# Optimization experiments

Measured on AMD Instinct MI355X. Metric: run time of the kernel, lower is better.

The kernel has to match this reference:

```python
import jax, jax.numpy as jnp
import numpy as np

N_HEADS = 8
EMBED_DIM = 512
HEAD_DIM = EMBED_DIM // N_HEADS
INPUT_DIM = 512


def setup_inputs() -> dict:
    key = jax.random.key(0)
    ks = jax.random.split(key, 9)
    B, N = 4, 2048
    s_in = 1.0 / np.sqrt(INPUT_DIM)
    s_e = 1.0 / np.sqrt(EMBED_DIM)
    return {
        "q": jax.random.normal(ks[0], (B, N, INPUT_DIM), dtype=jnp.float32),
        "wq": jax.random.uniform(ks[1], (EMBED_DIM, INPUT_DIM), jnp.float32, -s_in, s_in),
        "bq": jax.random.uniform(ks[2], (EMBED_DIM,), jnp.float32, -s_in, s_in),
        "wk": jax.random.uniform(ks[3], (EMBED_DIM, INPUT_DIM), jnp.float32, -s_in, s_in),
        "bk": jax.random.uniform(ks[4], (EMBED_DIM,), jnp.float32, -s_in, s_in),
        "wv": jax.random.uniform(ks[5], (EMBED_DIM, INPUT_DIM), jnp.float32, -s_in, s_in),
        "bv": jax.random.uniform(ks[6], (EMBED_DIM,), jnp.float32, -s_in, s_in),
        "wo": jax.random.uniform(ks[7], (EMBED_DIM, EMBED_DIM), jnp.float32, -s_e, s_e),
        "bo": jax.random.uniform(ks[8], (EMBED_DIM,), jnp.float32, -s_e, s_e),
    }


def reference(q, wq, bq, wk, bk, wv, bv, wo, bo):
    B, N, _ = q.shape
    # linear projections (torch Linear: x @ W.T + b)
    Q = (q @ wq.T + bq).reshape(B, N, N_HEADS, HEAD_DIM).transpose(0, 2, 1, 3)
    K = (q @ wk.T + bk).reshape(B, N, N_HEADS, HEAD_DIM).transpose(0, 2, 1, 3)
    V = (q @ wv.T + bv).reshape(B, N, N_HEADS, HEAD_DIM).transpose(0, 2, 1, 3)
    scores = jnp.einsum("bhqd,bhkd->bhqk", Q, K) / jnp.sqrt(
        jnp.asarray(HEAD_DIM, dtype=q.dtype)
    )
    weights = jax.nn.softmax(scores, axis=-1)
    out = jnp.einsum("bhqk,bhkd->bhqd", weights, V)  # [B,H,N,Dh]
    out = out.transpose(0, 2, 1, 3).reshape(B, N, EMBED_DIM)
    return out @ wo.T + bo
```

## Files before the change

### kernel.cpp

```cpp
#include <hip/hip_runtime.h>
#include <hip/hip_bf16.h>
#include <math.h>

#define SEQ    2048
#define DH     64
#define EMB    512
#define INDIM  512
#define NHEADS 8
#define BATCH  4
#define MTOT   (BATCH * SEQ)

typedef __attribute__((ext_vector_type(8))) short bf16x8;
typedef __attribute__((ext_vector_type(4))) float f32x4;

__device__ __forceinline__ ushort f2bf(float x) {
  union { float f; unsigned u; } v; v.f = x;
  unsigned r = v.u + 0x7FFFu + ((v.u >> 16) & 1u);
  return (ushort)(r >> 16);
}

__device__ __forceinline__ unsigned cvt_pk_bf16(float lo, float hi) {
  unsigned r;
  asm("v_cvt_pk_bf16_f32 %0, %1, %2" : "=v"(r) : "v"(lo), "v"(hi));
  return r;
}

__device__ __forceinline__ float fast_exp2(float x) {
  float r;
  asm("v_exp_f32 %0, %1" : "=v"(r) : "v"(x));
  return r;
}

__device__ __forceinline__ void permswap32(unsigned &x, unsigned &y) {
  asm("v_permlane32_swap_b32 %0, %1" : "+v"(x), "+v"(y));
}

__global__ __launch_bounds__(256) void conv_bf16(const float* __restrict__ src,
                                                 ushort* __restrict__ dst, int n8) {
  const int i = blockIdx.x * 256 + threadIdx.x;
  if (i >= n8) return;
  const float4 a = ((const float4*)src)[i * 2];
  const float4 b = ((const float4*)src)[i * 2 + 1];
  uint4 o;
  o.x = cvt_pk_bf16(a.x, a.y);
  o.y = cvt_pk_bf16(a.z, a.w);
  o.z = cvt_pk_bf16(b.x, b.y);
  o.w = cvt_pk_bf16(b.z, b.w);
  ((uint4*)dst)[i] = o;
}

__global__ __launch_bounds__(256) void conv_bf16_w4(
    const float* __restrict__ w0, const float* __restrict__ w1,
    const float* __restrict__ w2, const float* __restrict__ w3,
    ushort* __restrict__ dst, int n8per) {
  const int i = blockIdx.x * 256 + threadIdx.x;
  if (i >= n8per) return;
  const float* src = (blockIdx.y == 0) ? w0 : (blockIdx.y == 1) ? w1
                   : (blockIdx.y == 2) ? w2 : w3;
  ushort* d = dst + (size_t)blockIdx.y * n8per * 8;
  const float4 a = ((const float4*)src)[i * 2];
  const float4 b = ((const float4*)src)[i * 2 + 1];
  uint4 o;
  o.x = cvt_pk_bf16(a.x, a.y);
  o.y = cvt_pk_bf16(a.z, a.w);
  o.z = cvt_pk_bf16(b.x, b.y);
  o.w = cvt_pk_bf16(b.z, b.w);
  ((uint4*)d)[i] = o;
}

template <int MODE>
__global__ __launch_bounds__(256) void mfma_gemm(
    const ushort* __restrict__ A, const ushort* __restrict__ W,
    const float* __restrict__ b0, const float* __restrict__ b1,
    const float* __restrict__ b2,
    ushort* __restrict__ outQ, ushort* __restrict__ outK,
    ushort* __restrict__ outVT, float* __restrict__ outF) {
  __shared__ __align__(16) char smem[MODE == 0 ? 35840 : 16384];
  ushort* As = (ushort*)smem;
  ushort* Bs = (ushort*)(smem + 8192);
  ushort* Tl = (ushort*)smem;

  const int bm = blockIdx.x * 128;
  const int bn = blockIdx.y * 128;
  const int tid = threadIdx.x;
  const int wave = tid >> 6, lane = tid & 63;
  const int g = lane >> 4, ln = lane & 15;
  const int wr = wave >> 1, wc = wave & 1;

  f32x4 acc[4][4];
#pragma unroll
  for (int m = 0; m < 4; ++m)
#pragma unroll
    for (int n = 0; n < 4; ++n) acc[m][n] = (f32x4){0.f, 0.f, 0.f, 0.f};

  const size_t a_base = (size_t)(bm + wave * 16 + (lane >> 2)) * INDIM + (lane & 3) * 8;
  const size_t b_base = (size_t)(bn + wave * 16 + (lane >> 2)) * INDIM + (lane & 3) * 8;
  ushort* ldsA0 = As + wave * 512;
  ushort* ldsA1 = As + 2048 + wave * 512;
  ushort* ldsB0 = Bs + wave * 512;
  ushort* ldsB1 = Bs + 2048 + wave * 512;

  for (int k0 = 0; k0 < INDIM; k0 += 32) {
    __syncthreads();
    __builtin_amdgcn_global_load_lds(
        (const __attribute__((address_space(1))) void*)(A + a_base + k0),
        (__attribute__((address_space(3))) void*)ldsA0, 16, 0, 0);
    __builtin_amdgcn_global_load_lds(
        (const __attribute__((address_space(1))) void*)(A + a_base + 64 * INDIM + k0),
        (__attribute__((address_space(3))) void*)ldsA1, 16, 0, 0);
    __builtin_amdgcn_global_load_lds(
        (const __attribute__((address_space(1))) void*)(W + b_base + k0),
        (__attribute__((address_space(3))) void*)ldsB0, 16, 0, 0);
    __builtin_amdgcn_global_load_lds(
        (const __attribute__((address_space(1))) void*)(W + b_base + 64 * INDIM + k0),
        (__attribute__((address_space(3))) void*)ldsB1, 16, 0, 0);
    __syncthreads();

    bf16x8 af[4], bfv[4];
#pragma unroll
    for (int m = 0; m < 4; ++m)
      af[m] = *(const bf16x8*)&As[(64 * wr + 16 * m + ln) * 32 + 8 * g];
#pragma unroll
    for (int n = 0; n < 4; ++n)
      bfv[n] = *(const bf16x8*)&Bs[(64 * wc + 16 * n + ln) * 32 + 8 * g];
#pragma unroll
    for (int m = 0; m < 4; ++m)
#pragma unroll
      for (int n = 0; n < 4; ++n)
        acc[m][n] = __builtin_amdgcn_mfma_f32_16x16x32_bf16(af[m], bfv[n], acc[m][n], 0, 0, 0);
  }

  if (MODE == 1) {
#pragma unroll
    for (int n = 0; n < 4; ++n) {
      const int e = bn + 64 * wc + 16 * n + ln;
      const float bv = b0[e];
#pragma unroll
      for (int m = 0; m < 4; ++m)
#pragma unroll
        for (int r = 0; r < 4; ++r) {
          const int row = bm + 64 * wr + 16 * m + 4 * g + r;
          outF[(size_t)row * EMB + e] = acc[m][n][r] + bv;
        }
    }
    return;
  }

  const int which = bn >> 9;
  const float* bias = (which == 0) ? b0 : (which == 1) ? b1 : b2;

  if (which < 2) {
    const float scl = (which == 0) ? 0.18033688f : 1.0f;
    ushort* dst = (which == 0) ? outQ : outK;
#pragma unroll
    for (int n = 0; n < 4; ++n) {
      const int e = (bn & 511) + 64 * wc + 16 * n + ln;
      const float bv = bias[e];
      const int h = e >> 6, d = e & 63;
#pragma unroll
      for (int m = 0; m < 4; ++m)
#pragma unroll
        for (int r = 0; r < 4; ++r) {
          const int row = bm + 64 * wr + 16 * m + 4 * g + r;
          const int b = row >> 11, nn = row & (SEQ - 1);
          dst[(((size_t)(b * NHEADS + h) * SEQ) + nn) * DH + d] =
              f2bf((acc[m][n][r] + bv) * scl);
        }
    }
  } else {
    __syncthreads();
#pragma unroll
    for (int n = 0; n < 4; ++n) {
      const int cl = 64 * wc + 16 * n + ln;
      const float bv = bias[(bn & 511) + cl];
#pragma unroll
      for (int m = 0; m < 4; ++m)
#pragma unroll
        for (int r = 0; r < 4; ++r) {
          const int rl = 64 * wr + 16 * m + 4 * g + r;
          Tl[cl * 140 + rl] = f2bf(acc[m][n][r] + bv);
        }
    }
    __syncthreads();
    const int c = tid >> 1;
    const int rh = (tid & 1) * 64;
    const int e = (bn & 511) + c;
    const int h = e >> 6, d = e & 63;
    const int b = bm >> 11;
    const int nn0 = (bm & (SEQ - 1)) + rh;
    ushort* drow = outVT + (((size_t)(b * NHEADS + h) * DH) + d) * SEQ + nn0;
#pragma unroll
    for (int j = 0; j < 8; ++j)
      *(bf16x8*)&drow[j * 8] = *(const bf16x8*)&Tl[c * 140 + rh + j * 8];
  }
}

__global__ __launch_bounds__(256) void attn_mfma(const ushort* __restrict__ Q,
                                                 const ushort* __restrict__ K,
                                                 const ushort* __restrict__ VT,
                                                 ushort* __restrict__ O) {
  __shared__ __align__(16) ushort Kl[64 * 72];
  __shared__ __align__(16) ushort Vl[64 * 72];

  const int tid = threadIdx.x;
  const int wave = tid >> 6, lane = tid & 63;
  const int g = lane >> 4, ln = lane & 15;

  const int orig = blockIdx.x;
  const int swz = (orig & 7) * 64 + (orig >> 3);
  const int bh = swz >> 4;
  const int qx = swz & 15;
  const int qbase = qx * 128 + wave * 32;

  const ushort* Qb = Q + ((size_t)bh * SEQ + qbase) * DH;
  const ushort* Kb = K + (size_t)bh * SEQ * DH;
  const ushort* Vb = VT + (size_t)bh * DH * SEQ;

  const bf16x8 qfA0 = *(const bf16x8*)&Qb[ln * DH + 8 * g];
  const bf16x8 qfA1 = *(const bf16x8*)&Qb[ln * DH + 32 + 8 * g];
  const bf16x8 qfB0 = *(const bf16x8*)&Qb[(16 + ln) * DH + 8 * g];
  const bf16x8 qfB1 = *(const bf16x8*)&Qb[(16 + ln) * DH + 32 + 8 * g];

  f32x4 oaccA[4], oaccB[4];
#pragma unroll
  for (int t = 0; t < 4; ++t) {
    oaccA[t] = (f32x4){0.f, 0.f, 0.f, 0.f};
    oaccB[t] = (f32x4){0.f, 0.f, 0.f, 0.f};
  }
  float denomA = 0.f, denomB = 0.f;

  const int skv = tid >> 3, sd = (tid & 7) * 8;
  const int dt = tid >> 2, kc = (tid & 3) * 8;
  const int pr0 = skv ^ (((((skv >> 2) ^ (skv >> 3)) & 1)) * 12);
  const int s32 = skv + 32;
  const int pr1 = s32 ^ (((((s32 >> 2) ^ (s32 >> 3)) & 1)) * 12);

  bf16x8 k0v = *(const bf16x8*)&Kb[(size_t)skv * DH + sd];
  bf16x8 k1v = *(const bf16x8*)&Kb[(size_t)(32 + skv) * DH + sd];
  bf16x8 v0v = *(const bf16x8*)&Vb[(size_t)dt * SEQ + kc];
  bf16x8 v1v = *(const bf16x8*)&Vb[(size_t)dt * SEQ + 32 + kc];

  for (int kv0 = 0; kv0 < SEQ; kv0 += 64) {
    __syncthreads();
    *(bf16x8*)&Kl[pr0 * 72 + sd] = k0v;
    *(bf16x8*)&Kl[pr1 * 72 + sd] = k1v;
    *(bf16x8*)&Vl[dt * 72 + kc] = v0v;
    *(bf16x8*)&Vl[dt * 72 + 32 + kc] = v1v;

    const int nxt = (kv0 + 64 < SEQ) ? kv0 + 64 : kv0;
    k0v = *(const bf16x8*)&Kb[(size_t)(nxt + skv) * DH + sd];
    k1v = *(const bf16x8*)&Kb[(size_t)(nxt + 32 + skv) * DH + sd];
    v0v = *(const bf16x8*)&Vb[(size_t)dt * SEQ + nxt + kc];
    v1v = *(const bf16x8*)&Vb[(size_t)dt * SEQ + nxt + 32 + kc];

    asm volatile("s_waitcnt lgkmcnt(0)" ::: "memory");
    __builtin_amdgcn_s_barrier();

    bf16x8 ka[4][2], vb[2][4];
#pragma unroll
    for (int t = 0; t < 4; ++t) {
      ka[t][0] = *(const bf16x8*)&Kl[(16 * t + ln) * 72 + 8 * g];
      ka[t][1] = *(const bf16x8*)&Kl[(16 * t + ln) * 72 + 32 + 8 * g];
    }
#pragma unroll
    for (int c = 0; c < 2; ++c)
#pragma unroll
      for (int t = 0; t < 4; ++t)
        vb[c][t] = *(const bf16x8*)&Vl[(16 * t + ln) * 72 + 32 * c + 8 * g];

    {
      f32x4 s0 = (f32x4){0.f, 0.f, 0.f, 0.f};
      f32x4 s1 = s0, s2 = s0, s3 = s0;
      __builtin_amdgcn_s_setprio(1);
      s0 = __builtin_amdgcn_mfma_f32_16x16x32_bf16(ka[0][0], qfA0, s0, 0, 0, 0);
      s1 = __builtin_amdgcn_mfma_f32_16x16x32_bf16(ka[1][0], qfA0, s1, 0, 0, 0);
      s2 = __builtin_amdgcn_mfma_f32_16x16x32_bf16(ka[2][0], qfA0, s2, 0, 0, 0);
      s3 = __builtin_amdgcn_mfma_f32_16x16x32_bf16(ka[3][0], qfA0, s3, 0, 0, 0);
      s0 = __builtin_amdgcn_mfma_f32_16x16x32_bf16(ka[0][1], qfA1, s0, 0, 0, 0);
      s1 = __builtin_amdgcn_mfma_f32_16x16x32_bf16(ka[1][1], qfA1, s1, 0, 0, 0);
      s2 = __builtin_amdgcn_mfma_f32_16x16x32_bf16(ka[2][1], qfA1, s2, 0, 0, 0);
      s3 = __builtin_amdgcn_mfma_f32_16x16x32_bf16(ka[3][1], qfA1, s3, 0, 0, 0);
      __builtin_amdgcn_s_setprio(0);

      float p0[4], p1[4], p2[4], p3[4];
#pragma unroll
      for (int r = 0; r < 4; ++r) {
        p0[r] = fast_exp2(s0[r]);
        p1[r] = fast_exp2(s1[r]);
        p2[r] = fast_exp2(s2[r]);
        p3[r] = fast_exp2(s3[r]);
      }
      float ds = ((p0[0] + p0[1]) + (p0[2] + p0[3]))
               + ((p1[0] + p1[1]) + (p1[2] + p1[3]))
               + ((p2[0] + p2[1]) + (p2[2] + p2[3]))
               + ((p3[0] + p3[1]) + (p3[2] + p3[3]));
      ds += __shfl_xor(ds, 16);
      ds += __shfl_xor(ds, 32);
      denomA += ds;

      unsigned a0 = cvt_pk_bf16(p0[0], p0[1]);
      unsigned a2 = cvt_pk_bf16(p1[0], p1[1]);
      unsigned a1 = cvt_pk_bf16(p0[2], p0[3]);
      unsigned a3 = cvt_pk_bf16(p1[2], p1[3]);
      permswap32(a0, a2);
      permswap32(a1, a3);
      unsigned b0 = cvt_pk_bf16(p2[0], p2[1]);
      unsigned b2 = cvt_pk_bf16(p3[0], p3[1]);
      unsigned b1 = cvt_pk_bf16(p2[2], p2[3]);
      unsigned b3 = cvt_pk_bf16(p3[2], p3[3]);
      permswap32(b0, b2);
      permswap32(b1, b3);
      union { unsigned u[4]; bf16x8 v; } pa0, pa1;
      pa0.u[0] = a0; pa0.u[1] = a1; pa0.u[2] = a2; pa0.u[3] = a3;
      pa1.u[0] = b0; pa1.u[1] = b1; pa1.u[2] = b2; pa1.u[3] = b3;

      __builtin_amdgcn_s_setprio(1);
#pragma unroll
      for (int t = 0; t < 4; ++t) {
        oaccA[t] = __builtin_amdgcn_mfma_f32_16x16x32_bf16(pa0.v, vb[0][t], oaccA[t], 0, 0, 0);
        oaccA[t] = __builtin_amdgcn_mfma_f32_16x16x32_bf16(pa1.v, vb[1][t], oaccA[t], 0, 0, 0);
      }
      __builtin_amdgcn_s_setprio(0);
    }

    {
      f32x4 s0 = (f32x4){0.f, 0.f, 0.f, 0.f};
      f32x4 s1 = s0, s2 = s0, s3 = s0;
      __builtin_amdgcn_s_setprio(1);
      s0 = __builtin_amdgcn_mfma_f32_16x16x32_bf16(ka[0][0], qfB0, s0, 0, 0, 0);
      s1 = __builtin_amdgcn_mfma_f32_16x16x32_bf16(ka[1][0], qfB0, s1, 0, 0, 0);
      s2 = __builtin_amdgcn_mfma_f32_16x16x32_bf16(ka[2][0], qfB0, s2, 0, 0, 0);
      s3 = __builtin_amdgcn_mfma_f32_16x16x32_bf16(ka[3][0], qfB0, s3, 0, 0, 0);
      s0 = __builtin_amdgcn_mfma_f32_16x16x32_bf16(ka[0][1], qfB1, s0, 0, 0, 0);
      s1 = __builtin_amdgcn_mfma_f32_16x16x32_bf16(ka[1][1], qfB1, s1, 0, 0, 0);
      s2 = __builtin_amdgcn_mfma_f32_16x16x32_bf16(ka[2][1], qfB1, s2, 0, 0, 0);
      s3 = __builtin_amdgcn_mfma_f32_16x16x32_bf16(ka[3][1], qfB1, s3, 0, 0, 0);
      __builtin_amdgcn_s_setprio(0);

      float p0[4], p1[4], p2[4], p3[4];
#pragma unroll
      for (int r = 0; r < 4; ++r) {
        p0[r] = fast_exp2(s0[r]);
        p1[r] = fast_exp2(s1[r]);
        p2[r] = fast_exp2(s2[r]);
        p3[r] = fast_exp2(s3[r]);
      }
      float ds = ((p0[0] + p0[1]) + (p0[2] + p0[3]))
               + ((p1[0] + p1[1]) + (p1[2] + p1[3]))
               + ((p2[0] + p2[1]) + (p2[2] + p2[3]))
               + ((p3[0] + p3[1]) + (p3[2] + p3[3]));
      ds += __shfl_xor(ds, 16);
      ds += __shfl_xor(ds, 32);
      denomB += ds;

      unsigned a0 = cvt_pk_bf16(p0[0], p0[1]);
      unsigned a2 = cvt_pk_bf16(p1[0], p1[1]);
      unsigned a1 = cvt_pk_bf16(p0[2], p0[3]);
      unsigned a3 = cvt_pk_bf16(p1[2], p1[3]);
      permswap32(a0, a2);
      permswap32(a1, a3);
      unsigned b0 = cvt_pk_bf16(p2[0], p2[1]);
      unsigned b2 = cvt_pk_bf16(p3[0], p3[1]);
      unsigned b1 = cvt_pk_bf16(p2[2], p2[3]);
      unsigned b3 = cvt_pk_bf16(p3[2], p3[3]);
      permswap32(b0, b2);
      permswap32(b1, b3);
      union { unsigned u[4]; bf16x8 v; } pa0, pa1;
      pa0.u[0] = a0; pa0.u[1] = a1; pa0.u[2] = a2; pa0.u[3] = a3;
      pa1.u[0] = b0; pa1.u[1] = b1; pa1.u[2] = b2; pa1.u[3] = b3;

      __builtin_amdgcn_s_setprio(1);
#pragma unroll
      for (int t = 0; t < 4; ++t) {
        oaccB[t] = __builtin_amdgcn_mfma_f32_16x16x32_bf16(pa0.v, vb[0][t], oaccB[t], 0, 0, 0);
        oaccB[t] = __builtin_amdgcn_mfma_f32_16x16x32_bf16(pa1.v, vb[1][t], oaccB[t], 0, 0, 0);
      }
      __builtin_amdgcn_s_setprio(0);
    }
  }

  const float invA = 1.0f / denomA;
  const float invB = 1.0f / denomB;
  const int b = bh >> 3, h = bh & 7;
#pragma unroll
  for (int r = 0; r < 4; ++r) {
    const float irA = __shfl(invA, 4 * g + r);
    const float irB = __shfl(invB, 4 * g + r);
    ushort* opA = O + ((size_t)(b * SEQ) + qbase + 4 * g + r) * EMB + h * 64;
    ushort* opB = O + ((size_t)(b * SEQ) + qbase + 16 + 4 * g + r) * EMB + h * 64;
#pragma unroll
    for (int t = 0; t < 4; ++t) {
      opA[16 * t + ln] = f2bf(oaccA[t][r] * irA);
      opB[16 * t + ln] = f2bf(oaccB[t][r] * irB);
    }
  }
}

extern "C" void kernel_launch(void* const* d_in, const int* in_sizes, int n_in,
                              void* d_out, int out_size, void* d_ws, size_t ws_size,
                              hipStream_t stream) {
  const float* q  = (const float*)d_in[0];
  const float* wq = (const float*)d_in[1];
  const float* bq = (const float*)d_in[2];
  const float* wk = (const float*)d_in[3];
  const float* bk = (const float*)d_in[4];
  const float* wv = (const float*)d_in[5];
  const float* bv = (const float*)d_in[6];
  const float* wo = (const float*)d_in[7];
  const float* bo = (const float*)d_in[8];
  float* out = (float*)d_out;

  const size_t XSZ = (size_t)MTOT * INDIM;
  const size_t WSZ = (size_t)EMB * INDIM;
  const size_t QSZ = (size_t)BATCH * NHEADS * SEQ * DH;
  ushort* wsX = (ushort*)d_ws;
  ushort* wsW = wsX + XSZ;
  ushort* wsQ = wsW + 4 * WSZ;
  ushort* wsK = wsQ + QSZ;
  ushort* wsVT = wsK + QSZ;
  ushort* wsA = wsVT + QSZ;

  const dim3 blk(256);

  conv_bf16<<<dim3(XSZ / 8 / 256), blk, 0, stream>>>(q, wsX, XSZ / 8);
  conv_bf16_w4<<<dim3(WSZ / 8 / 256, 4), blk, 0, stream>>>(wq, wk, wv, wo, wsW, WSZ / 8);

  mfma_gemm<0><<<dim3(MTOT / 128, 1536 / 128), blk, 0, stream>>>(
      wsX, wsW, bq, bk, bv, wsQ, wsK, wsVT, nullptr);

  attn_mfma<<<dim3(512), blk, 0, stream>>>(wsQ, wsK, wsVT, wsA);

  mfma_gemm<1><<<dim3(MTOT / 128, EMB / 128), blk, 0, stream>>>(
      wsA, wsW + 3 * WSZ, bo, nullptr, nullptr, nullptr, nullptr, nullptr, out);
}
```

Measured before the change: 107.6 us.

## Double-buffer K/V LDS tiles and compute softmax denominator via MFMA with ones

Splits the K/V shared-memory tiles into two buffers so the next tile is written to LDS while the current one is consumed, which drops one barrier per iteration. The row-sum of the softmax numerators is now taken by extra MFMAs against a vector of bf16 ones, replacing the VALU adds and cross-lane shuffles. The trade-off is twice the LDS use, which may reduce occupancy, two more MFMAs per half-step, and a denominator summed from bf16-rounded probabilities, which now matches the weights the numerator uses.

```diff
diff --git a/kernel.cpp b/kernel.cpp
--- a/kernel.cpp
+++ b/kernel.cpp
@@ -199,8 +199,8 @@
                                                  const ushort* __restrict__ K,
                                                  const ushort* __restrict__ VT,
                                                  ushort* __restrict__ O) {
-  __shared__ __align__(16) ushort Kl[64 * 72];
-  __shared__ __align__(16) ushort Vl[64 * 72];
+  __shared__ __align__(16) ushort Kl[2][64 * 72];
+  __shared__ __align__(16) ushort Vl[2][64 * 72];
 
   const int tid = threadIdx.x;
   const int wave = tid >> 6, lane = tid & 63;
@@ -221,13 +221,18 @@
   const bf16x8 qfB0 = *(const bf16x8*)&Qb[(16 + ln) * DH + 8 * g];
   const bf16x8 qfB1 = *(const bf16x8*)&Qb[(16 + ln) * DH + 32 + 8 * g];
 
+  bf16x8 vones;
+#pragma unroll
+  for (int i = 0; i < 8; ++i) vones[i] = (short)0x3F80;
+
   f32x4 oaccA[4], oaccB[4];
+  f32x4 oaccDA = (f32x4){0.f, 0.f, 0.f, 0.f};
+  f32x4 oaccDB = (f32x4){0.f, 0.f, 0.f, 0.f};
 #pragma unroll
   for (int t = 0; t < 4; ++t) {
     oaccA[t] = (f32x4){0.f, 0.f, 0.f, 0.f};
     oaccB[t] = (f32x4){0.f, 0.f, 0.f, 0.f};
   }
-  float denomA = 0.f, denomB = 0.f;
 
   const int skv = tid >> 3, sd = (tid & 7) * 8;
   const int dt = tid >> 2, kc = (tid & 3) * 8;
@@ -239,34 +244,49 @@
   bf16x8 k1v = *(const bf16x8*)&Kb[(size_t)(32 + skv) * DH + sd];
   bf16x8 v0v = *(const bf16x8*)&Vb[(size_t)dt * SEQ + kc];
   bf16x8 v1v = *(const bf16x8*)&Vb[(size_t)dt * SEQ + 32 + kc];
-
-  for (int kv0 = 0; kv0 < SEQ; kv0 += 64) {
-    __syncthreads();
-    *(bf16x8*)&Kl[pr0 * 72 + sd] = k0v;
-    *(bf16x8*)&Kl[pr1 * 72 + sd] = k1v;
-    *(bf16x8*)&Vl[dt * 72 + kc] = v0v;
-    *(bf16x8*)&Vl[dt * 72 + 32 + kc] = v1v;
-
-    const int nxt = (kv0 + 64 < SEQ) ? kv0 + 64 : kv0;
-    k0v = *(const bf16x8*)&Kb[(size_t)(nxt + skv) * DH + sd];
-    k1v = *(const bf16x8*)&Kb[(size_t)(nxt + 32 + skv) * DH + sd];
-    v0v = *(const bf16x8*)&Vb[(size_t)dt * SEQ + nxt + kc];
-    v1v = *(const bf16x8*)&Vb[(size_t)dt * SEQ + nxt + 32 + kc];
-
-    asm volatile("s_waitcnt lgkmcnt(0)" ::: "memory");
-    __builtin_amdgcn_s_barrier();
+  *(bf16x8*)&Kl[0][pr0 * 72 + sd] = k0v;
+  *(bf16x8*)&Kl[0][pr1 * 72 + sd] = k1v;
+  *(bf16x8*)&Vl[0][dt * 72 + kc] = v0v;
+  *(bf16x8*)&Vl[0][dt * 72 + 32 + kc] = v1v;
+  k0v = *(const bf16x8*)&Kb[(size_t)(64 + skv) * DH + sd];
+  k1v = *(const bf16x8*)&Kb[(size_t)(96 + skv) * DH + sd];
+  v0v = *(const bf16x8*)&Vb[(size_t)dt * SEQ + 64 + kc];
+  v1v = *(const bf16x8*)&Vb[(size_t)dt * SEQ + 96 + kc];
+  asm volatile("s_waitcnt lgkmcnt(0)" ::: "memory");
+  __builtin_amdgcn_s_barrier();
+
+  for (int it = 0; it < 32; ++it) {
+    const int cur = it & 1;
+    ushort* Kc = Kl[cur];
+    ushort* Vc = Vl[cur];
+
+    if (it < 31) {
+      ushort* Kn = Kl[cur ^ 1];
+      ushort* Vn = Vl[cur ^ 1];
+      *(bf16x8*)&Kn[pr0 * 72 + sd] = k0v;
+      *(bf16x8*)&Kn[pr1 * 72 + sd] = k1v;
+      *(bf16x8*)&Vn[dt * 72 + kc] = v0v;
+      *(bf16x8*)&Vn[dt * 72 + 32 + kc] = v1v;
+    }
+    {
+      const int nxt = (it + 2 < 32) ? (it + 2) * 64 : 31 * 64;
+      k0v = *(const bf16x8*)&Kb[(size_t)(nxt + skv) * DH + sd];
+      k1v = *(const bf16x8*)&Kb[(size_t)(nxt + 32 + skv) * DH + sd];
+      v0v = *(const bf16x8*)&Vb[(size_t)dt * SEQ + nxt + kc];
+      v1v = *(const bf16x8*)&Vb[(size_t)dt * SEQ + nxt + 32 + kc];
+    }
 
     bf16x8 ka[4][2], vb[2][4];
 #pragma unroll
     for (int t = 0; t < 4; ++t) {
-      ka[t][0] = *(const bf16x8*)&Kl[(16 * t + ln) * 72 + 8 * g];
-      ka[t][1] = *(const bf16x8*)&Kl[(16 * t + ln) * 72 + 32 + 8 * g];
+      ka[t][0] = *(const bf16x8*)&Kc[(16 * t + ln) * 72 + 8 * g];
+      ka[t][1] = *(const bf16x8*)&Kc[(16 * t + ln) * 72 + 32 + 8 * g];
     }
 #pragma unroll
     for (int c = 0; c < 2; ++c)
 #pragma unroll
       for (int t = 0; t < 4; ++t)
-        vb[c][t] = *(const bf16x8*)&Vl[(16 * t + ln) * 72 + 32 * c + 8 * g];
+        vb[c][t] = *(const bf16x8*)&Vc[(16 * t + ln) * 72 + 32 * c + 8 * g];
 
     {
       f32x4 s0 = (f32x4){0.f, 0.f, 0.f, 0.f};
@@ -290,13 +310,6 @@
         p2[r] = fast_exp2(s2[r]);
         p3[r] = fast_exp2(s3[r]);
       }
-      float ds = ((p0[0] + p0[1]) + (p0[2] + p0[3]))
-               + ((p1[0] + p1[1]) + (p1[2] + p1[3]))
-               + ((p2[0] + p2[1]) + (p2[2] + p2[3]))
-               + ((p3[0] + p3[1]) + (p3[2] + p3[3]));
-      ds += __shfl_xor(ds, 16);
-      ds += __shfl_xor(ds, 32);
-      denomA += ds;
 
       unsigned a0 = cvt_pk_bf16(p0[0], p0[1]);
       unsigned a2 = cvt_pk_bf16(p1[0], p1[1]);
@@ -320,6 +333,8 @@
         oaccA[t] = __builtin_amdgcn_mfma_f32_16x16x32_bf16(pa0.v, vb[0][t], oaccA[t], 0, 0, 0);
         oaccA[t] = __builtin_amdgcn_mfma_f32_16x16x32_bf16(pa1.v, vb[1][t], oaccA[t], 0, 0, 0);
       }
+      oaccDA = __builtin_amdgcn_mfma_f32_16x16x32_bf16(pa0.v, vones, oaccDA, 0, 0, 0);
+      oaccDA = __builtin_amdgcn_mfma_f32_16x16x32_bf16(pa1.v, vones, oaccDA, 0, 0, 0);
       __builtin_amdgcn_s_setprio(0);
     }
 
@@ -345,13 +360,6 @@
         p2[r] = fast_exp2(s2[r]);
         p3[r] = fast_exp2(s3[r]);
       }
-      float ds = ((p0[0] + p0[1]) + (p0[2] + p0[3]))
-               + ((p1[0] + p1[1]) + (p1[2] + p1[3]))
-               + ((p2[0] + p2[1]) + (p2[2] + p2[3]))
-               + ((p3[0] + p3[1]) + (p3[2] + p3[3]));
-      ds += __shfl_xor(ds, 16);
-      ds += __shfl_xor(ds, 32);
-      denomB += ds;
 
       unsigned a0 = cvt_pk_bf16(p0[0], p0[1]);
       unsigned a2 = cvt_pk_bf16(p1[0], p1[1]);
@@ -375,17 +383,20 @@
         oaccB[t] = __builtin_amdgcn_mfma_f32_16x16x32_bf16(pa0.v, vb[0][t], oaccB[t], 0, 0, 0);
         oaccB[t] = __builtin_amdgcn_mfma_f32_16x16x32_bf16(pa1.v, vb[1][t], oaccB[t], 0, 0, 0);
       }
+      oaccDB = __builtin_amdgcn_mfma_f32_16x16x32_bf16(pa0.v, vones, oaccDB, 0, 0, 0);
+      oaccDB = __builtin_amdgcn_mfma_f32_16x16x32_bf16(pa1.v, vones, oaccDB, 0, 0, 0);
       __builtin_amdgcn_s_setprio(0);
     }
-  }
-
-  const float invA = 1.0f / denomA;
-  const float invB = 1.0f / denomB;
+
+    asm volatile("s_waitcnt lgkmcnt(0)" ::: "memory");
+    __builtin_amdgcn_s_barrier();
+  }
+
   const int b = bh >> 3, h = bh & 7;
 #pragma unroll
   for (int r = 0; r < 4; ++r) {
-    const float irA = __shfl(invA, 4 * g + r);
-    const float irB = __shfl(invB, 4 * g + r);
+    const float irA = 1.0f / oaccDA[r];
+    const float irB = 1.0f / oaccDB[r];
     ushort* opA = O + ((size_t)(b * SEQ) + qbase + 4 * g + r) * EMB + h * 64;
     ushort* opB = O + ((size_t)(b * SEQ) + qbase + 16 + 4 * g + r) * EMB + h * 64;
 #pragma unroll
```

After: 103.4 us. 3.9% less time.
